# Kernel tuning notes

Hardware: AMD Instinct MI355X
Metric: run time of the kernel (lower is better)

## Reference

```python
import jax, jax.numpy as jnp
import numpy as np

N = 12288
D = 64
K = 16
EPS = 1e-5
DIAG_BIAS = 1e6


def setup_inputs() -> dict:
    key = jax.random.key(0)
    k1, k2 = jax.random.split(key)
    coords = jax.random.normal(k1, (N, D), dtype=jnp.float32)
    potential = jax.random.normal(k2, (N,), dtype=jnp.float32)
    return {"coords": coords, "potential": potential, "k": K}


def reference(coords, potential, k):
    # Pairwise squared distances: ||xi - xj||^2 + eps  (same math as (diff**2).sum(-1))
    sq = jnp.sum(coords * coords, axis=1)                      # (N,)
    dist2 = sq[:, None] + sq[None, :] - 2.0 * (coords @ coords.T) + EPS  # (N, N)
    n = coords.shape[0]
    dist2 = dist2 + jnp.eye(n, dtype=coords.dtype) * DIAG_BIAS  # exclude self
    # kNN via top-k of negated distances (matches torch.topk(-dist2, k, dim=1))
    knn_vals, knn_idx = jax.lax.top_k(-dist2, k)                # (N, k) each
    sigma2 = jnp.mean(dist2)                                    # scalar (incl. diag bias, as in source)
    weights = jnp.exp(knn_vals / (sigma2 + EPS))                # (N, k)
    v_nb = potential[knn_idx]                                   # (N, k) gather
    lap = jnp.sum(weights * (v_nb - potential[:, None]), axis=1)  # (N,)
    return lap
```

## Files before the change

kernel.cpp:

```cpp
#include <hip/hip_runtime.h>
#include <hip/hip_bf16.h>

#define N_PTS 12288
#define DIM   64
#define KSEL  16
#define EPS_F 1e-5f
#define TMARGIN 2.0f

typedef __bf16 bf16x8 __attribute__((ext_vector_type(8)));
typedef float  f32x16 __attribute__((ext_vector_type(16)));

__device__ __forceinline__ void grid_sync(int* bar)
{
    __syncthreads();
    if (threadIdx.x == 0) {
        __hip_atomic_fetch_add(bar, 1, __ATOMIC_RELEASE, __HIP_MEMORY_SCOPE_AGENT);
        while (__hip_atomic_load(bar, __ATOMIC_ACQUIRE, __HIP_MEMORY_SCOPE_AGENT)
               < (int)gridDim.x)
            __builtin_amdgcn_s_sleep(2);
    }
    __syncthreads();
}

template<int CVN>
__device__ __forceinline__ void rank_core(const unsigned* __restrict__ drow,
                                          int S, int l32, int* __restrict__ fj)
{
    unsigned cv[CVN]; int rk[CVN];
    #pragma unroll
    for (int t = 0; t < CVN; ++t) {
        cv[t] = (t * 32 + l32 < S) ? drow[t * 32 + l32] : 0xFFFFFFFFu;
        rk[t] = 0;
    }
    #pragma unroll 4
    for (int m = 0; m < S; ++m) {
        const unsigned o = drow[m];
        #pragma unroll
        for (int t = 0; t < CVN; ++t) rk[t] += (o < cv[t]) ? 1 : 0;
    }
    #pragma unroll
    for (int t = 0; t < CVN; ++t)
        if (rk[t] < 32 && cv[t] != 0xFFFFFFFFu)
            fj[rk[t]] = (int)(cv[t] & 0x3FFFu);
}

__global__ __launch_bounds__(512) void mega_kernel(
    const float* __restrict__ coords,
    const float* __restrict__ pot,
    float* __restrict__ s1,
    float* __restrict__ sx,
    int* __restrict__ bar,
    __hip_bfloat16* __restrict__ chi,
    __hip_bfloat16* __restrict__ chiX,
    float* __restrict__ out)
{
    constexpr int ROWS = 48, DCAP = 256, DPAD = 257;
    constexpr int JSL  = N_PTS / 8;
    constexpr int STEPS = JSL / 32;

    __shared__ float    colsh[8][64];
    __shared__ float    sqs8[8];
    __shared__ float    sqloc[ROWS];
    __shared__ float    pool[ROWS][32];
    __shared__ float    TrowS[ROWS];
    __shared__ unsigned dense[ROWS * DPAD];
    __shared__ int      cnt[ROWS];
    __shared__ int      finj[16][32];
    __shared__ double   refd[16][32];
    __shared__ double   s_inv_den;

    const int tid  = threadIdx.x;
    const int lane = tid & 63;
    const int wave = tid >> 6;
    const int l31  = lane & 31;
    const int half = lane >> 5;
    const int ibase = (int)blockIdx.x * ROWS;

    float colsum = 0.f, sqsum = 0.f;
    #pragma unroll 1
    for (int k = 0; k < 6; ++k) {
        const int rl = wave * 6 + k, gr = ibase + rl;
        const float x = coords[gr * DIM + lane];
        chi[gr * DIM + lane] = __float2bfloat16(x);
        colsum += x;
        float p = x * x;
        #pragma unroll
        for (int off = 32; off > 0; off >>= 1) p += __shfl_xor(p, off, 64);
        if (lane == 0) { sqloc[rl] = p; sqsum += p; }
        if (lane < 16) {
            __hip_bfloat16 v = __float2bfloat16(0.0f);
            if (lane == 0)      v = __float2bfloat16(p);
            else if (lane == 1) {
                const float h = (float)__float2bfloat16(p);
                v = __float2bfloat16(p - h);
            }
            else if (lane < 4)  v = __float2bfloat16(1.0f);
            chiX[gr * 16 + lane] = v;
        }
    }
    colsh[wave][lane] = colsum;
    if (lane == 0) sqs8[wave] = sqsum;
    if (tid < ROWS) cnt[tid] = 0;
    __syncthreads();
    if (wave == 0) {
        float c = 0.f;
        #pragma unroll
        for (int w8 = 0; w8 < 8; ++w8) c += colsh[w8][lane];
        atomicAdd(&sx[lane], c);
    }
    if (tid == 0) {
        float t = 0.f;
        #pragma unroll
        for (int w8 = 0; w8 < 8; ++w8) t += sqs8[w8];
        atomicAdd(s1, t);
    }
    grid_sync(bar);

    if (tid == 0) {
        double S1 = (double)s1[0], m2 = 0.0;
        for (int d = 0; d < DIM; ++d) { double t = (double)sx[d]; m2 += t * t; }
        const double NN = (double)N_PTS;
        s_inv_den = 1.0 / ((2.0 * NN * S1 - 2.0 * m2) / (NN * NN)
                           + 1e-5 + 1e6 / NN + 1e-5);
    }

    const bf16x8* cp  = (const bf16x8*)chi;
    const bf16x8* cpX = (const bf16x8*)chiX;
    bf16x8 zf;
    #pragma unroll
    for (int e = 0; e < 8; ++e) zf[e] = (__bf16)0.0f;

    bf16x8 Bf[2][5];
    const int  i0r = ibase + l31;
    const bool t1v = (l31 < 16);
    const int  i1r = ibase + 32 + (l31 & 15);
    #pragma unroll
    for (int m = 0; m < 4; ++m) {
        Bf[0][m] = cp[i0r * 8 + 2 * m + half];
        Bf[1][m] = t1v ? cp[i1r * 8 + 2 * m + half] : zf;
    }
    {
        bf16x8 v = zf;
        if (half == 0) {
            const float bs = sqloc[l31] + EPS_F;
            const __bf16 bh = (__bf16)(0.5f * bs);
            const __bf16 bl = (__bf16)(0.5f * bs - (float)bh);
            v[0] = (__bf16)(-0.5f); v[1] = (__bf16)(-0.5f);
            v[2] = (__bf16)(-(float)bh); v[3] = (__bf16)(-(float)bl);
        }
        Bf[0][4] = v;
        v = zf;
        if (half == 0 && t1v) {
            const float bs = sqloc[32 + l31] + EPS_F;
            const __bf16 bh = (__bf16)(0.5f * bs);
            const __bf16 bl = (__bf16)(0.5f * bs - (float)bh);
            v[0] = (__bf16)(-0.5f); v[1] = (__bf16)(-0.5f);
            v[2] = (__bf16)(-(float)bh); v[3] = (__bf16)(-(float)bl);
        }
        Bf[1][4] = v;
    }

    const int jw = wave * JSL;
    const f32x16 Z = {0.f,0.f,0.f,0.f,0.f,0.f,0.f,0.f,
                      0.f,0.f,0.f,0.f,0.f,0.f,0.f,0.f};

    auto LDA = [&](int s, bf16x8 (&A)[5]) {
        const int jr = jw + s * 32 + l31;
        A[0] = cp[jr * 8 + half];
        A[1] = cp[jr * 8 + 2 + half];
        A[2] = cp[jr * 8 + 4 + half];
        A[3] = cp[jr * 8 + 6 + half];
        A[4] = cpX[jr * 2 + half];
    };
    auto ACC2 = [&](const bf16x8 (&A)[5], f32x16& a0, f32x16& a1) {
        a0 = __builtin_amdgcn_mfma_f32_32x32x16_bf16(A[0], Bf[0][0], Z, 0, 0, 0);
        a1 = __builtin_amdgcn_mfma_f32_32x32x16_bf16(A[0], Bf[1][0], Z, 0, 0, 0);
        #pragma unroll
        for (int m = 1; m < 5; ++m) {
            a0 = __builtin_amdgcn_mfma_f32_32x32x16_bf16(A[m], Bf[0][m], a0, 0, 0, 0);
            a1 = __builtin_amdgcn_mfma_f32_32x32x16_bf16(A[m], Bf[1][m], a1, 0, 0, 0);
        }
    };

    float p00 = -1e30f, p01 = -1e30f, p10 = -1e30f, p11 = -1e30f;
    auto TOP2 = [&](const f32x16& a, float& m0, float& m1) {
        #pragma unroll
        for (int r = 0; r < 16; ++r) {
            const float v = a[r];
            const bool g = v > m0;
            m1 = g ? m0 : fmaxf(m1, v);
            m0 = fmaxf(m0, v);
        }
    };
    {
        bf16x8 Aa[5], Ab[5];
        LDA(0, Aa); LDA(4, Ab);
        #pragma unroll 1
        for (int k = 0; k < 12; k += 2) {
            { f32x16 a0, a1; ACC2(Aa, a0, a1);
              int sn = (k + 2) * 4; LDA(sn < STEPS ? sn : 0, Aa);
              TOP2(a0, p00, p01); TOP2(a1, p10, p11); }
            { f32x16 a0, a1; ACC2(Ab, a0, a1);
              int sn = (k + 3) * 4; LDA(sn < STEPS ? sn : 0, Ab);
              TOP2(a0, p00, p01); TOP2(a1, p10, p11); }
        }
    }
    {
        const int slot = wave * 4 + half * 2;
        pool[l31][slot]     = -2.f * p00;
        pool[l31][slot + 1] = -2.f * p01;
        if (t1v) {
            pool[32 + l31][slot]     = -2.f * p10;
            pool[32 + l31][slot + 1] = -2.f * p11;
        }
    }
    __syncthreads();

    const int hw  = tid >> 5;
    const int l32 = tid & 31;
    #pragma unroll 1
    for (int pass = 0; pass < 3; ++pass) {
        const int row = pass * 16 + hw;
        const float val = pool[row][l32];
        int rank = 0;
        #pragma unroll 8
        for (int m = 0; m < 32; ++m) {
            const float o = pool[row][m];
            rank += (o < val || (o == val && m < l32)) ? 1 : 0;
        }
        if (rank == 16) TrowS[row] = val + TMARGIN;
    }
    __syncthreads();

    const float tthr0 = -0.5f * TrowS[l31];
    const float tthr1 = t1v ? -0.5f * TrowS[32 + l31] : 1e30f;

    auto EPI = [&](int s, const f32x16& a, float tthr, int lrow) {
        float mx = fmaxf(fmaxf(fmaxf(a[0], a[1]), fmaxf(a[2], a[3])),
                         fmaxf(fmaxf(a[4], a[5]), fmaxf(a[6], a[7])));
        mx = fmaxf(mx, fmaxf(fmaxf(fmaxf(a[8], a[9]),  fmaxf(a[10], a[11])),
                             fmaxf(fmaxf(a[12], a[13]), fmaxf(a[14], a[15]))));
        if (mx > tthr) {
            const int jb = jw + s * 32 + 4 * half;
            #pragma unroll
            for (int r = 0; r < 16; ++r) {
                if (a[r] > tthr) {
                    const float d2 = -2.f * a[r];
                    const unsigned pk = (__float_as_uint(d2) & 0xFFFFC000u)
                                      | (unsigned)(jb + (r & 3) + 8 * (r >> 2));
                    const int idx = atomicAdd(&cnt[lrow], 1);
                    if (idx < DCAP) dense[lrow * DPAD + idx] = pk;
                }
            }
        }
    };
    {
        bf16x8 Aa[5], Ab[5];
        LDA(0, Aa); LDA(1, Ab);
        #pragma unroll 1
        for (int s = 0; s < STEPS; s += 2) {
            { f32x16 a0, a1; ACC2(Aa, a0, a1);
              int sn = s + 2; LDA(sn < STEPS ? sn : 0, Aa);
              EPI(s, a0, tthr0, l31); EPI(s, a1, tthr1, 32 + (l31 & 15)); }
            { f32x16 a0, a1; ACC2(Ab, a0, a1);
              int sn = s + 3; LDA(sn < STEPS ? sn : 0, Ab);
              EPI(s + 1, a0, tthr0, l31); EPI(s + 1, a1, tthr1, 32 + (l31 & 15)); }
        }
    }
    __syncthreads();

    const double inv_den = s_inv_den;
    #pragma unroll 1
    for (int pass = 0; pass < 3; ++pass) {
        const int row  = pass * 16 + hw;
        const int grow = ibase + row;
        int S = cnt[row]; S = S < DCAP ? S : DCAP;
        finj[hw][l32] = grow;

        const unsigned* drow = dense + row * DPAD;
        if (S <= 96) rank_core<3>(drow, S, l32, finj[hw]);
        else         rank_core<8>(drow, S, l32, finj[hw]);
        __syncthreads();

        const int j = finj[hw][l32];
        const float4* xi = (const float4*)(coords + grow * DIM);
        const float4* xj = (const float4*)(coords + j * DIM);
        double dot = 0.0, sqi = 0.0, sqj = 0.0;
        #pragma unroll
        for (int q = 0; q < DIM / 4; ++q) {
            const float4 a = xi[q], b = xj[q];
            dot += (double)a.x * (double)b.x + (double)a.y * (double)b.y
                 + (double)a.z * (double)b.z + (double)a.w * (double)b.w;
            sqi += (double)a.x * (double)a.x + (double)a.y * (double)a.y
                 + (double)a.z * (double)a.z + (double)a.w * (double)a.w;
            sqj += (double)b.x * (double)b.x + (double)b.y * (double)b.y
                 + (double)b.z * (double)b.z + (double)b.w * (double)b.w;
        }
        double d2 = sqi + sqj + 1e-5 - 2.0 * dot;
        if (j == grow) d2 = 1e300;
        refd[hw][l32] = d2;
        __syncthreads();

        int rank = 0;
        #pragma unroll 1
        for (int m = 0; m < 32; ++m) {
            const double o = refd[hw][m];
            rank += (o < d2 || (o == d2 && m < l32)) ? 1 : 0;
        }
        const double wgt = exp(-d2 * inv_den);
        double contrib = (rank < KSEL && j != grow)
                       ? wgt * ((double)pot[j] - (double)pot[grow]) : 0.0;
        #pragma unroll
        for (int off = 1; off < 32; off <<= 1)
            contrib += __shfl_xor(contrib, off, 64);
        if (l32 == 0) out[grow] = (float)contrib;
        __syncthreads();
    }
}

extern "C" void kernel_launch(void* const* d_in, const int* in_sizes, int n_in,
                              void* d_out, int out_size, void* d_ws, size_t ws_size,
                              hipStream_t stream)
{
    (void)in_sizes; (void)n_in; (void)out_size; (void)ws_size;
    const float* coords = (const float*)d_in[0];
    const float* pot    = (const float*)d_in[1];

    char* w = (char*)d_ws;
    float* s1 = (float*)w;
    float* sx = (float*)(w + 4);
    int*   bar = (int*)(w + 512);
    __hip_bfloat16* chi  = (__hip_bfloat16*)(w + 1024);
    __hip_bfloat16* chiX = (__hip_bfloat16*)(w + 1024 + (size_t)N_PTS * DIM * 2);

    hipMemsetAsync((void*)w, 0, 1024, stream);
    mega_kernel<<<dim3(N_PTS / 48), dim3(512), 0, stream>>>(
        coords, pot, s1, sx, bar, chi, chiX, (float*)d_out);
}
```

Before: 237.1 us.

## Replace per-candidate LDS atomics with per-thread candidate buffers and prefix compaction

The GEMM epilogue no longer does an LDS atomicAdd on a per-row counter for every candidate that passes the threshold. Each thread now writes candidates into a private strided LDS buffer with a per-thread count, spilling to an atomic overflow list only past a fixed capacity. After the loop, per-segment counts are prefix-summed to compact the candidates into the dense per-row arrays. This removes atomic contention from the hot loop, at the cost of more LDS, an extra compaction phase with syncs, a changed stored value (raw accumulator rather than scaled distance, which is order-equivalent), and a larger rank_core instantiation.

```diff
diff --git a/kernel.cpp b/kernel.cpp
--- a/kernel.cpp
+++ b/kernel.cpp
@@ -54,7 +54,9 @@
     __hip_bfloat16* __restrict__ chiX,
     float* __restrict__ out)
 {
-    constexpr int ROWS = 48, DCAP = 256, DPAD = 257;
+    constexpr int ROWS = 48, CAPP = 12, OCAP = 96;
+    constexpr int DCAP = 16 * CAPP + OCAP;
+    constexpr int DPAD = DCAP + 1;
     constexpr int JSL  = N_PTS / 8;
     constexpr int STEPS = JSL / 32;
 
@@ -63,8 +65,12 @@
     __shared__ float    sqloc[ROWS];
     __shared__ float    pool[ROWS][32];
     __shared__ float    TrowS[ROWS];
+    __shared__ unsigned buf[2 * CAPP * 512];
+    __shared__ int      cntT[2][16][32];
     __shared__ unsigned dense[ROWS * DPAD];
-    __shared__ int      cnt[ROWS];
+    __shared__ unsigned ovf[ROWS][OCAP];
+    __shared__ int      ovcnt[ROWS];
+    __shared__ int      stotS[ROWS];
     __shared__ int      finj[16][32];
     __shared__ double   refd[16][32];
     __shared__ double   s_inv_den;
@@ -100,7 +106,7 @@
     }
     colsh[wave][lane] = colsum;
     if (lane == 0) sqs8[wave] = sqsum;
-    if (tid < ROWS) cnt[tid] = 0;
+    if (tid < ROWS) ovcnt[tid] = 0;
     __syncthreads();
     if (wave == 0) {
         float c = 0.f;
@@ -234,23 +240,25 @@
 
     const float tthr0 = -0.5f * TrowS[l31];
     const float tthr1 = t1v ? -0.5f * TrowS[32 + l31] : 1e30f;
-
-    auto EPI = [&](int s, const f32x16& a, float tthr, int lrow) {
-        float mx = fmaxf(fmaxf(fmaxf(a[0], a[1]), fmaxf(a[2], a[3])),
-                         fmaxf(fmaxf(a[4], a[5]), fmaxf(a[6], a[7])));
-        mx = fmaxf(mx, fmaxf(fmaxf(fmaxf(a[8], a[9]),  fmaxf(a[10], a[11])),
-                             fmaxf(fmaxf(a[12], a[13]), fmaxf(a[14], a[15]))));
-        if (mx > tthr) {
-            const int jb = jw + s * 32 + 4 * half;
-            #pragma unroll
-            for (int r = 0; r < 16; ++r) {
-                if (a[r] > tthr) {
-                    const float d2 = -2.f * a[r];
-                    const unsigned pk = (__float_as_uint(d2) & 0xFFFFC000u)
-                                      | (unsigned)(jb + (r & 3) + 8 * (r >> 2));
-                    const int idx = atomicAdd(&cnt[lrow], 1);
-                    if (idx < DCAP) dense[lrow * DPAD + idx] = pk;
-                }
+    const int   row1  = 32 + (l31 & 15);
+
+    int ct0 = 0, ct1 = 0;
+    auto EPI = [&](int s, const f32x16& a0, const f32x16& a1) {
+        const int jb = jw + s * 32 + 4 * half;
+        #pragma unroll
+        for (int r = 0; r < 16; ++r) {
+            const unsigned joff = (unsigned)(jb + (r & 3) + 8 * (r >> 2));
+            if (a0[r] > tthr0) {
+                const unsigned pk = (__float_as_uint(a0[r]) & 0xFFFFC000u) | joff;
+                if (ct0 < CAPP) { buf[ct0 * 512 + tid] = pk; ++ct0; }
+                else { const int sl = atomicAdd(&ovcnt[l31], 1);
+                       if (sl < OCAP) ovf[l31][sl] = pk; }
+            }
+            if (a1[r] > tthr1) {
+                const unsigned pk = (__float_as_uint(a1[r]) & 0xFFFFC000u) | joff;
+                if (ct1 < CAPP) { buf[(CAPP + ct1) * 512 + tid] = pk; ++ct1; }
+                else { const int sl = atomicAdd(&ovcnt[row1], 1);
+                       if (sl < OCAP) ovf[row1][sl] = pk; }
             }
         }
     };
@@ -261,11 +269,46 @@
         for (int s = 0; s < STEPS; s += 2) {
             { f32x16 a0, a1; ACC2(Aa, a0, a1);
               int sn = s + 2; LDA(sn < STEPS ? sn : 0, Aa);
-              EPI(s, a0, tthr0, l31); EPI(s, a1, tthr1, 32 + (l31 & 15)); }
+              EPI(s, a0, a1); }
             { f32x16 a0, a1; ACC2(Ab, a0, a1);
               int sn = s + 3; LDA(sn < STEPS ? sn : 0, Ab);
-              EPI(s + 1, a0, tthr0, l31); EPI(s + 1, a1, tthr1, 32 + (l31 & 15)); }
-        }
+              EPI(s + 1, a0, a1); }
+        }
+    }
+    const int seg = wave * 2 + half;
+    cntT[0][seg][l31] = ct0;
+    if (t1v) cntT[1][seg][l31] = ct1;
+    __syncthreads();
+
+    {
+        int b0 = 0, b1 = 0;
+        #pragma unroll 4
+        for (int sg = 0; sg < 16; ++sg) {
+            if (sg < seg) {
+                b0 += cntT[0][sg][l31];
+                b1 += cntT[1][sg][l31 & 15];
+            }
+        }
+        for (int p = 0; p < ct0; ++p)
+            dense[l31 * DPAD + b0 + p] = buf[p * 512 + tid];
+        if (t1v)
+            for (int p = 0; p < ct1; ++p)
+                dense[row1 * DPAD + b1 + p] = buf[(CAPP + p) * 512 + tid];
+    }
+    __syncthreads();
+    if (wave == 0 && tid < ROWS) {
+        const int row = tid;
+        int tot = 0;
+        if (row < 32) {
+            #pragma unroll 4
+            for (int sg = 0; sg < 16; ++sg) tot += cntT[0][sg][row];
+        } else {
+            #pragma unroll 4
+            for (int sg = 0; sg < 16; ++sg) tot += cntT[1][sg][row - 32];
+        }
+        const int ov = ovcnt[row] < OCAP ? ovcnt[row] : OCAP;
+        for (int o = 0; o < ov; ++o) dense[row * DPAD + tot + o] = ovf[row][o];
+        stotS[row] = tot + ov;
     }
     __syncthreads();
 
@@ -274,12 +317,12 @@
     for (int pass = 0; pass < 3; ++pass) {
         const int row  = pass * 16 + hw;
         const int grow = ibase + row;
-        int S = cnt[row]; S = S < DCAP ? S : DCAP;
+        const int S    = stotS[row];
         finj[hw][l32] = grow;
 
         const unsigned* drow = dense + row * DPAD;
         if (S <= 96) rank_core<3>(drow, S, l32, finj[hw]);
-        else         rank_core<8>(drow, S, l32, finj[hw]);
+        else         rank_core<9>(drow, S, l32, finj[hw]);
         __syncthreads();
 
         const int j = finj[hw][l32];
```

Result: no change. 234.2 us (-1.2%).
